# Performance work log

Hardware: AMD Instinct MI355X
Metric: run time of the kernel (lower is better)

## Reference

```python
import jax, jax.numpy as jnp
import numpy as np

B, EMBED, H, W = 16, 256, 64, 64
HEADS, POINTS = 8, 4  # mmcv MultiScaleDeformableAttention defaults, num_levels=1


def make_pe(d, h, w):
    # LoFTR-style PositionEncodingSine: pe[0::4]=sin(x*div), pe[1::4]=cos(x*div),
    # pe[2::4]=sin(y*div), pe[3::4]=cos(y*div); x,y are 1-based cumsum positions.
    y = jnp.broadcast_to(jnp.arange(1, h + 1, dtype=jnp.float32)[:, None], (h, w))
    x = jnp.broadcast_to(jnp.arange(1, w + 1, dtype=jnp.float32)[None, :], (h, w))
    div = jnp.exp(jnp.arange(0, d // 2, 2, dtype=jnp.float32) * (-np.log(10000.0) / (d // 2)))
    div = div[:, None, None]  # (d//4,1,1)
    pe = jnp.stack([jnp.sin(x * div), jnp.cos(x * div), jnp.sin(y * div), jnp.cos(y * div)], axis=1)
    return pe.reshape(d, h, w)[None]  # (1,d,h,w)


def reference_points(h, w):
    # Faithful to original: meshgrid(linspace(0,1,W), linspace(0,1,H), indexing='ij'),
    # stack (col, row), flatten -> (W*H, 2)
    gx, gy = jnp.meshgrid(jnp.linspace(0.0, 1.0, w), jnp.linspace(0.0, 1.0, h), indexing='ij')
    return jnp.stack([gy, gx], -1).reshape(-1, 2)


def reference(query, value, W_off, b_off, W_attn, b_attn, W_val, b_val, W_out, b_out):
    Bq, C, h, w = query.shape
    N = h * w
    d = C // HEADS
    pe = make_pe(C, h, w)
    q = query + pe  # query += self.pe(query)
    q_flat = q.reshape(Bq, C, N).transpose(0, 2, 1)      # (B,N,C)
    v_flat = value.reshape(Bq, C, N).transpose(0, 2, 1)  # (B,N,C)
    # value projection, split heads: (B,heads,N,d) -- spatial index n = y*w + x
    v = (v_flat @ W_val.T + b_val).reshape(Bq, N, HEADS, d).transpose(0, 2, 1, 3)
    off = (q_flat @ W_off.T + b_off).reshape(Bq, N, HEADS, POINTS, 2)
    attn = jax.nn.softmax((q_flat @ W_attn.T + b_attn).reshape(Bq, N, HEADS, POINTS), axis=-1)
    ref = reference_points(h, w)                          # (N,2)
    normalizer = jnp.array([w, h], jnp.float32)           # (W, H) per mmcv
    loc = ref[None, :, None, None, :] + off / normalizer  # (B,N,heads,P,2) in [0,1]
    grid = 2.0 * loc - 1.0                                # grid_sample coords, align_corners=False
    sx = grid[..., 0].transpose(0, 2, 1, 3).reshape(Bq, HEADS, N * POINTS)
    sy = grid[..., 1].transpose(0, 2, 1, 3).reshape(Bq, HEADS, N * POINTS)
    ix = (sx + 1.0) * w * 0.5 - 0.5
    iy = (sy + 1.0) * h * 0.5 - 0.5
    x0f = jnp.floor(ix); y0f = jnp.floor(iy)
    wx = ix - x0f; wy = iy - y0f
    x0 = x0f.astype(jnp.int32); y0 = y0f.astype(jnp.int32)

    def gather(yi, xi):
        # zero padding outside the image
        valid = (xi >= 0) & (xi < w) & (yi >= 0) & (yi < h)
        idx = jnp.clip(yi, 0, h - 1) * w + jnp.clip(xi, 0, w - 1)  # (B,heads,M)
        g = jnp.take_along_axis(v, idx[..., None], axis=2)          # (B,heads,M,d)
        return g * valid[..., None]

    samp = (((1 - wx) * (1 - wy))[..., None] * gather(y0, x0)
            + (wx * (1 - wy))[..., None] * gather(y0, x0 + 1)
            + ((1 - wx) * wy)[..., None] * gather(y0 + 1, x0)
            + (wx * wy)[..., None] * gather(y0 + 1, x0 + 1))        # (B,heads,N*P,d)
    samp = samp.reshape(Bq, HEADS, N, POINTS, d)
    attn_t = attn.transpose(0, 2, 1, 3)                             # (B,heads,N,P)
    out = jnp.einsum('bhnp,bhnpd->bnhd', attn_t, samp).reshape(Bq, N, C)
    out = out @ W_out.T + b_out + q_flat  # mmcv internal identity residual (dropout in eval = id)
    out = out.transpose(0, 2, 1).reshape(Bq, C, h, w)
    return out + q  # outer residual: output + query (query already has pe added)


def setup_inputs():
    key = jax.random.key(0)
    ks = jax.random.split(key, 8)
    s = 0.02
    return {
        'query': jax.random.normal(ks[0], (B, EMBED, H, W), jnp.float32),
        'value': jax.random.normal(ks[1], (B, EMBED, H, W), jnp.float32),
        'W_off': jax.random.normal(ks[2], (HEADS * POINTS * 2, EMBED), jnp.float32) * s,
        'b_off': jax.random.normal(ks[3], (HEADS * POINTS * 2,), jnp.float32) * 2.0,
        'W_attn': jax.random.normal(ks[4], (HEADS * POINTS, EMBED), jnp.float32) * s,
        'b_attn': jnp.zeros((HEADS * POINTS,), jnp.float32),
        'W_val': jax.random.normal(ks[5], (EMBED, EMBED), jnp.float32) * s,
        'b_val': jnp.zeros((EMBED,), jnp.float32),
        'W_out': jax.random.normal(ks[6], (EMBED, EMBED), jnp.float32) * s,
        'b_out': jnp.zeros((EMBED,), jnp.float32),
    }
```

## Files before the change

kernel.cpp:

```cpp
#include <hip/hip_runtime.h>
#include <hip/hip_bf16.h>

typedef __bf16 bf16;
typedef bf16 bf16x8 __attribute__((ext_vector_type(8)));
typedef bf16 bf16x4 __attribute__((ext_vector_type(4)));
typedef float f32x4 __attribute__((ext_vector_type(4)));

#define CB 16
#define CC 256
#define CH 64
#define CW 64
#define CN 4096
#define NHEADS 8
#define NPOINTS 4
#define HDIM 32
#define TBP 132

#define MFMA16(a, b, c) __builtin_amdgcn_mfma_f32_16x16x32_bf16(a, b, c, 0, 0, 0)

__device__ __forceinline__ void gload16(const void* g, void* l) {
    __builtin_amdgcn_global_load_lds((const __attribute__((address_space(1))) void*)g,
                                     (__attribute__((address_space(3))) void*)l, 16, 0, 0);
}

__global__ __launch_bounds__(256) void pe_pack(float* __restrict__ pe,
                                               const float* __restrict__ Wv,
                                               const float* __restrict__ Woff,
                                               const float* __restrict__ Wattn,
                                               const float* __restrict__ Wout,
                                               bf16* __restrict__ Wv_bf,
                                               bf16* __restrict__ W96_bf,
                                               bf16* __restrict__ Wout_bf) {
    int idx = blockIdx.x * 256 + threadIdx.x;
    if (idx < CC * CN) {
        int c = idx >> 12, n = idx & (CN - 1);
        int r = n >> 6, x = n & 63;
        int i = c >> 2, t = c & 3;
        float div = __expf(-logf(10000.0f) * (float)i / 64.0f);
        float arg = ((t < 2) ? (float)(x + 1) : (float)(r + 1)) * div;
        pe[idx] = (t & 1) ? cosf(arg) : sinf(arg);
    }
    if (idx < CC * CC) {
        Wv_bf[idx] = (bf16)Wv[idx];
        Wout_bf[idx] = (bf16)Wout[idx];
    }
    if (idx < 96 * CC) {
        W96_bf[idx] = (bf16)((idx < 64 * CC) ? Woff[idx] : Wattn[idx - 64 * CC]);
    }
}

__global__ __launch_bounds__(256) void vproj_g(const float* __restrict__ value,
                                               const bf16* __restrict__ Wv,
                                               const float* __restrict__ bv,
                                               bf16* __restrict__ v_s) {
    __shared__ __align__(16) char smem[17408];
    float* T = (float*)smem;
    const int TP = 66;

    int tid = threadIdx.x, lane = tid & 63, wave = tid >> 6;
    int wm = wave >> 1, wn = wave & 1, g = lane >> 4, lr = lane & 15;
    int n0 = blockIdx.x * 64, m0 = blockIdx.y * 128, b = blockIdx.z;
    int nl = tid & 63, kg = tid >> 6;
    const float* src = value + (size_t)b * CC * CN + n0 + nl;

    float v[16];
#pragma unroll
    for (int p = 0; p < 16; ++p) v[p] = src[(size_t)(kg * 16 + p) * CN];

    f32x4 acc[4][2] = {};
    for (int t = 0; t < 4; ++t) {
#pragma unroll
        for (int half = 0; half < 2; ++half) {
            bf16x8 o;
#pragma unroll
            for (int p = 0; p < 8; ++p) o[p] = (bf16)v[half * 8 + p];
            int slot = (kg * 2 + half) ^ (nl & 7);
            *(bf16x8*)(smem + (t & 1) * 8192 + nl * 128 + slot * 16) = o;
        }
        __syncthreads();
        if (t < 3) {
#pragma unroll
            for (int p = 0; p < 16; ++p)
                v[p] = src[(size_t)((t + 1) * 64 + kg * 16 + p) * CN];
        }
#pragma unroll
        for (int ks = 0; ks < 2; ++ks) {
            bf16x8 af[4], bfr[2];
#pragma unroll
            for (int mf = 0; mf < 4; ++mf)
                af[mf] = *(const bf16x8*)&Wv[(size_t)(m0 + wm * 64 + mf * 16 + lr) * CC + t * 64 + ks * 32 + g * 8];
#pragma unroll
            for (int nf = 0; nf < 2; ++nf) {
                int row = wn * 32 + nf * 16 + lr;
                bfr[nf] = *(const bf16x8*)(smem + (t & 1) * 8192 + row * 128 + (((ks * 4 + g) ^ (row & 7)) * 16));
            }
#pragma unroll
            for (int mf = 0; mf < 4; ++mf)
#pragma unroll
                for (int nf = 0; nf < 2; ++nf)
                    acc[mf][nf] = MFMA16(af[mf], bfr[nf], acc[mf][nf]);
        }
    }

#pragma unroll
    for (int pass = 0; pass < 2; ++pass) {
        __syncthreads();
        if (wm == pass) {
#pragma unroll
            for (int mf = 0; mf < 4; ++mf)
#pragma unroll
                for (int nf = 0; nf < 2; ++nf)
#pragma unroll
                    for (int i = 0; i < 4; ++i)
                        T[(mf * 16 + g * 4 + i) * TP + wn * 32 + nf * 16 + lr] = acc[mf][nf][i];
        }
        __syncthreads();
#pragma unroll
        for (int it = 0; it < 2; ++it) {
            int item = it * 256 + tid;
            int qg = item & 7, n_l = item >> 3;
            int cg = m0 + pass * 64 + qg * 8;
            int head = cg >> 5, dd0 = cg & 31;
            bf16x8 o;
#pragma unroll
            for (int u = 0; u < 8; ++u)
                o[u] = (bf16)(T[(qg * 8 + u) * TP + n_l] + bv[cg + u]);
            *(bf16x8*)&v_s[(((size_t)b * NHEADS + head) * CN + n0 + n_l) * HDIM + dd0] = o;
        }
    }
}

__global__ __launch_bounds__(256, 4) void offattn_sample(const float* __restrict__ query,
                                                         const float* __restrict__ pe,
                                                         const bf16* __restrict__ W96,
                                                         const float* __restrict__ boff,
                                                         const float* __restrict__ battn,
                                                         const bf16* __restrict__ v_s,
                                                         bf16* __restrict__ s) {
    __shared__ __align__(16) char smem[33792];
    float* ot = (float*)smem;
    unsigned* tbl = (unsigned*)smem;

    int tid = threadIdx.x, lane = tid & 63, wave = tid >> 6;
    int wm = wave >> 1, wn = wave & 1, g = lane >> 4, lr = lane & 15;
    int id = blockIdx.x;
    int xcd = id & 7, local = id >> 3;
    int b = xcd * 2 + (local >> 6);
    int nt = local & 63;
    int n0 = nt * 64;
    int nl = tid & 63, kg = tid >> 6;
    const float* qs = query + (size_t)b * CC * CN + n0 + nl;
    const float* ps = pe + n0 + nl;

    float v[16];
#pragma unroll
    for (int p = 0; p < 16; ++p) {
        size_t off = (size_t)(kg * 16 + p) * CN;
        v[p] = __builtin_nontemporal_load(&qs[off]) + ps[off];
    }
    asm volatile("" ::: "memory");

    f32x4 acc[3][2] = {};
    for (int t = 0; t < 4; ++t) {
#pragma unroll
        for (int half = 0; half < 2; ++half) {
            bf16x8 o;
#pragma unroll
            for (int p = 0; p < 8; ++p) o[p] = (bf16)v[half * 8 + p];
            int slot = (kg * 2 + half) ^ (nl & 7);
            *(bf16x8*)(smem + (t & 1) * 8192 + nl * 128 + slot * 16) = o;
        }
        __syncthreads();
        if (t < 3) {
#pragma unroll
            for (int p = 0; p < 16; ++p) {
                size_t off = (size_t)((t + 1) * 64 + kg * 16 + p) * CN;
                v[p] = __builtin_nontemporal_load(&qs[off]) + ps[off];
            }
            asm volatile("" ::: "memory");
        }
#pragma unroll
        for (int ks = 0; ks < 2; ++ks) {
            bf16x8 af[3], bfr[2];
#pragma unroll
            for (int mf = 0; mf < 3; ++mf)
                af[mf] = *(const bf16x8*)&W96[(size_t)(wm * 48 + mf * 16 + lr) * CC + t * 64 + ks * 32 + g * 8];
#pragma unroll
            for (int nf = 0; nf < 2; ++nf) {
                int row = wn * 32 + nf * 16 + lr;
                bfr[nf] = *(const bf16x8*)(smem + (t & 1) * 8192 + row * 128 + (((ks * 4 + g) ^ (row & 7)) * 16));
            }
#pragma unroll
            for (int mf = 0; mf < 3; ++mf)
#pragma unroll
                for (int nf = 0; nf < 2; ++nf)
                    acc[mf][nf] = MFMA16(af[mf], bfr[nf], acc[mf][nf]);
        }
    }
    __syncthreads();

#pragma unroll
    for (int mf = 0; mf < 3; ++mf) {
#pragma unroll
        for (int i = 0; i < 4; ++i) {
            int j = wm * 48 + mf * 16 + g * 4 + i;
            float bias = (j < 64) ? boff[j] : battn[j - 64];
#pragma unroll
            for (int nf = 0; nf < 2; ++nf) {
                int col = wn * 32 + nf * 16 + lr;
                ot[j * 65 + col] = acc[mf][nf][i] + bias;
            }
        }
    }
    __syncthreads();

    unsigned pk[2][16];
#pragma unroll
    for (int it = 0; it < 2; ++it) {
        int item = it * 256 + tid;
        int inl = item & 63, h = item >> 6;
        float lg0 = ot[(64 + h * 4 + 0) * 65 + inl];
        float lg1 = ot[(64 + h * 4 + 1) * 65 + inl];
        float lg2 = ot[(64 + h * 4 + 2) * 65 + inl];
        float lg3 = ot[(64 + h * 4 + 3) * 65 + inl];
        float m = fmaxf(fmaxf(lg0, lg1), fmaxf(lg2, lg3));
        float e0 = __expf(lg0 - m), e1 = __expf(lg1 - m);
        float e2 = __expf(lg2 - m), e3 = __expf(lg3 - m);
        float inv = 1.0f / (e0 + e1 + e2 + e3);
        float ep[4] = {e0, e1, e2, e3};
#pragma unroll
        for (int p = 0; p < NPOINTS; ++p) {
            float off0 = ot[(h * 8 + p * 2 + 0) * 65 + inl];
            float off1 = ot[(h * 8 + p * 2 + 1) * 65 + inl];
            float ix = (float)inl * (64.0f / 63.0f) + off0 - 0.5f;
            float iy = (float)nt * (64.0f / 63.0f) + off1 - 0.5f;
            float x0f = floorf(ix), y0f = floorf(iy);
            float wx = ix - x0f, wy = iy - y0f;
            int x0 = (int)x0f, y0 = (int)y0f;
            int x1 = x0 + 1, y1 = y0 + 1;
            float vx0 = (x0 >= 0 && x0 < CW) ? 1.f : 0.f;
            float vx1 = (x1 >= 0 && x1 < CW) ? 1.f : 0.f;
            float vy0 = (y0 >= 0 && y0 < CH) ? 1.f : 0.f;
            float vy1 = (y1 >= 0 && y1 < CH) ? 1.f : 0.f;
            int x0c = min(max(x0, 0), CW - 1), x1c = min(max(x1, 0), CW - 1);
            int y0c = min(max(y0, 0), CH - 1), y1c = min(max(y1, 0), CH - 1);
            float a = ep[p] * inv;
            float w00 = a * (1.f - wx) * (1.f - wy) * vx0 * vy0;
            float w01 = a * wx * (1.f - wy) * vx1 * vy0;
            float w10 = a * (1.f - wx) * wy * vx0 * vy1;
            float w11 = a * wx * wy * vx1 * vy1;
            unsigned c00 = (unsigned)(y0c * CW + x0c), c01 = (unsigned)(y0c * CW + x1c);
            unsigned c10 = (unsigned)(y1c * CW + x0c), c11 = (unsigned)(y1c * CW + x1c);
            pk[it][p * 4 + 0] = ((unsigned)__builtin_bit_cast(unsigned short, (_Float16)w00) << 16) | c00;
            pk[it][p * 4 + 1] = ((unsigned)__builtin_bit_cast(unsigned short, (_Float16)w01) << 16) | c01;
            pk[it][p * 4 + 2] = ((unsigned)__builtin_bit_cast(unsigned short, (_Float16)w10) << 16) | c10;
            pk[it][p * 4 + 3] = ((unsigned)__builtin_bit_cast(unsigned short, (_Float16)w11) << 16) | c11;
        }
    }
    __syncthreads();
#pragma unroll
    for (int it = 0; it < 2; ++it) {
        int item = it * 256 + tid;
        int inl = item & 63, h = item >> 6;
        uint4* dst = (uint4*)(tbl + inl * TBP + h * 16);
#pragma unroll
        for (int j = 0; j < 4; ++j) {
            uint4 w4;
            w4.x = pk[it][j * 4 + 0]; w4.y = pk[it][j * 4 + 1];
            w4.z = pk[it][j * 4 + 2]; w4.w = pk[it][j * 4 + 3];
            dst[j] = w4;
        }
    }
    __syncthreads();

    int q = tid & 3, h2 = (tid >> 2) & 7, ng = tid >> 5;
    const bf16* vb = v_s + (((size_t)b * NHEADS + h2) * CN) * HDIM + q * 8;
#pragma unroll
    for (int iter = 0; iter < 8; ++iter) {
        int snl = iter * 8 + ng;
        const uint4* tb4 = (const uint4*)(tbl + snl * TBP + h2 * 16);
        unsigned ue[16];
#pragma unroll
        for (int j = 0; j < 4; ++j) {
            uint4 t4 = tb4[j];
            ue[j * 4 + 0] = t4.x; ue[j * 4 + 1] = t4.y;
            ue[j * 4 + 2] = t4.z; ue[j * 4 + 3] = t4.w;
        }
        asm volatile("" ::: "memory");
        bf16x8 gr[16];
#pragma unroll
        for (int e = 0; e < 16; ++e)
            gr[e] = *(const bf16x8*)&vb[(int)(ue[e] & 0xFFFu) * HDIM];
        asm volatile("" ::: "memory");
        float a0 = 0.f, a1 = 0.f, a2 = 0.f, a3 = 0.f;
        float a4 = 0.f, a5 = 0.f, a6 = 0.f, a7 = 0.f;
#pragma unroll
        for (int e = 0; e < 16; ++e) {
            float w = (float)__builtin_bit_cast(_Float16, (unsigned short)(ue[e] >> 16));
            a0 += w * (float)gr[e][0]; a1 += w * (float)gr[e][1];
            a2 += w * (float)gr[e][2]; a3 += w * (float)gr[e][3];
            a4 += w * (float)gr[e][4]; a5 += w * (float)gr[e][5];
            a6 += w * (float)gr[e][6]; a7 += w * (float)gr[e][7];
        }
        bf16x8 o;
        o[0] = (bf16)a0; o[1] = (bf16)a1; o[2] = (bf16)a2; o[3] = (bf16)a3;
        o[4] = (bf16)a4; o[5] = (bf16)a5; o[6] = (bf16)a6; o[7] = (bf16)a7;
        *(bf16x8*)&s[((size_t)b * CN + n0 + snl) * CC + h2 * 32 + q * 8] = o;
    }
}

__global__ __launch_bounds__(256) void outproj_v8(const bf16* __restrict__ s_t,
                                                  const bf16* __restrict__ Wout,
                                                  const float* __restrict__ bout,
                                                  const float* __restrict__ query,
                                                  const float* __restrict__ pe,
                                                  float* __restrict__ out) {
    __shared__ __align__(16) char smem[33792];
    float* T = (float*)smem;
    const int TP = 132;

    int tid = threadIdx.x, lane = tid & 63, wave = tid >> 6;
    int wm = wave >> 1, wn = wave & 1, g = lane >> 4, lr = lane & 15;
    int id = blockIdx.x;
    int swz = (id & 7) * 128 + (id >> 3);
    int n0 = (swz & 31) * 128, c0 = ((swz >> 5) & 1) * 128, b = swz >> 6;
    const bf16* sb = s_t + ((size_t)b * CN + n0) * CC;

    int rloc = lane >> 2, sl = lane & 3;

    auto stage = [&](int t, int bsel) {
#pragma unroll
        for (int j = 0; j < 2; ++j) {
            int cidx = wave * 2 + j;
            int row = cidx * 16 + rloc;
            int chunk = sl ^ (row & 3);
            const bf16* gA = sb + (size_t)row * CC + t * 32 + chunk * 8;
            const bf16* gB = Wout + (size_t)(c0 + row) * CC + t * 32 + chunk * 8;
            gload16(gA, smem + bsel * 16384 + cidx * 1024);
            gload16(gB, smem + bsel * 16384 + 8192 + cidx * 1024);
        }
    };

    stage(0, 0);

    f32x4 acc[4][4] = {};
    for (int t = 0; t < 8; ++t) {
        __syncthreads();
        if (t < 7) stage(t + 1, (t + 1) & 1);
        bf16x8 af[4], bfr[4];
#pragma unroll
        for (int mf = 0; mf < 4; ++mf) {
            int row = wm * 64 + mf * 16 + lr;
            af[mf] = *(const bf16x8*)(smem + (t & 1) * 16384 + row * 64 + ((g ^ (row & 3)) * 16));
        }
#pragma unroll
        for (int nf = 0; nf < 4; ++nf) {
            int row = wn * 64 + nf * 16 + lr;
            bfr[nf] = *(const bf16x8*)(smem + (t & 1) * 16384 + 8192 + row * 64 + ((g ^ (row & 3)) * 16));
        }
#pragma unroll
        for (int mf = 0; mf < 4; ++mf)
#pragma unroll
            for (int nf = 0; nf < 4; ++nf)
                acc[mf][nf] = MFMA16(af[mf], bfr[nf], acc[mf][nf]);
    }
    __syncthreads();

    int lr5 = tid & 31, rq = tid >> 5;
#pragma unroll
    for (int ch = 0; ch < 2; ++ch) {
        if (wn == ch) {
#pragma unroll
            for (int mf = 0; mf < 4; ++mf)
#pragma unroll
                for (int nf = 0; nf < 4; ++nf) {
                    int cl = nf * 16 + lr;
                    int nl = wm * 64 + mf * 16 + g * 4;
                    *(f32x4*)&T[cl * TP + nl] = acc[mf][nf];
                }
        }
        __syncthreads();
#pragma unroll
        for (int pass = 0; pass < 8; ++pass) {
            int cl = pass * 8 + rq;
            int c = c0 + ch * 64 + cl;
            int n = n0 + lr5 * 4;
            f32x4 v = *(const f32x4*)&T[cl * TP + lr5 * 4];
            size_t base = ((size_t)b * CC + c) * CN + n;
            f32x4 q4 = *(const f32x4*)&query[base];
            f32x4 p4 = *(const f32x4*)&pe[(size_t)c * CN + n];
            float bias = bout[c];
#pragma unroll
            for (int j = 0; j < 4; ++j) v[j] = v[j] + bias + 2.0f * (q4[j] + p4[j]);
            *(f32x4*)&out[base] = v;
        }
        __syncthreads();
    }
}

extern "C" void kernel_launch(void* const* d_in, const int* in_sizes, int n_in,
                              void* d_out, int out_size, void* d_ws, size_t ws_size,
                              hipStream_t stream) {
    const float* query = (const float*)d_in[0];
    const float* value = (const float*)d_in[1];
    const float* W_off = (const float*)d_in[2];
    const float* b_off = (const float*)d_in[3];
    const float* W_attn = (const float*)d_in[4];
    const float* b_attn = (const float*)d_in[5];
    const float* W_val = (const float*)d_in[6];
    const float* b_val = (const float*)d_in[7];
    const float* W_out = (const float*)d_in[8];
    const float* b_out = (const float*)d_in[9];
    float* out = (float*)d_out;

    char* p = (char*)d_ws;
    float* pe = (float*)p;            p += (size_t)CC * CN * 4;
    bf16* Wv_bf = (bf16*)p;           p += (size_t)CC * CC * 2;
    bf16* Wout_bf = (bf16*)p;         p += (size_t)CC * CC * 2;
    bf16* W96_bf = (bf16*)p;          p += (size_t)96 * CC * 2 + 256;
    bf16* v_s = (bf16*)p;             p += (size_t)CB * NHEADS * CN * HDIM * 2;
    bf16* s_t = (bf16*)p;             p += (size_t)CB * CN * CC * 2;

    pe_pack<<<dim3((CC * CN + 255) / 256), dim3(256), 0, stream>>>(pe, W_val, W_off, W_attn,
                                                                   W_out, Wv_bf, W96_bf, Wout_bf);
    vproj_g<<<dim3(CN / 64, 2, CB), dim3(256), 0, stream>>>(value, Wv_bf, b_val, v_s);
    offattn_sample<<<dim3(1024), dim3(256), 0, stream>>>(query, pe, W96_bf,
                                                         b_off, b_attn, v_s, s_t);
    outproj_v8<<<dim3(1024), dim3(256), 0, stream>>>(s_t, Wout_bf, b_out, query, pe, out);
}
```

Baseline: 136.4 us.

## Merge value projection with offset/attention compute; split sampling into separate kernel

The value projection and the offset/attention-weight projection now run in one launch, selected by blockIdx.y, so the two independent GEMMs can execute concurrently on the GPU. The packed bilinear sampling table is written to a global buffer instead of shared memory, and a new kernel does the gather-and-accumulate sampling. This removes the serialization between the value projection and the offset computation. In exchange it adds a 32 MB global table that must be written and read back, plus an extra kernel launch.

```diff
diff --git a/kernel.cpp b/kernel.cpp
--- a/kernel.cpp
+++ b/kernel.cpp
@@ -14,7 +14,6 @@
 #define NHEADS 8
 #define NPOINTS 4
 #define HDIM 32
-#define TBP 132
 
 #define MFMA16(a, b, c) __builtin_amdgcn_mfma_f32_16x16x32_bf16(a, b, c, 0, 0, 0)
 
@@ -49,104 +48,98 @@
     }
 }
 
-__global__ __launch_bounds__(256) void vproj_g(const float* __restrict__ value,
-                                               const bf16* __restrict__ Wv,
-                                               const float* __restrict__ bv,
-                                               bf16* __restrict__ v_s) {
-    __shared__ __align__(16) char smem[17408];
-    float* T = (float*)smem;
-    const int TP = 66;
-
+__global__ __launch_bounds__(256) void vproj_oa(const float* __restrict__ value,
+                                                const bf16* __restrict__ Wv,
+                                                const float* __restrict__ bv,
+                                                bf16* __restrict__ v_s,
+                                                const float* __restrict__ query,
+                                                const float* __restrict__ pe,
+                                                const bf16* __restrict__ W96,
+                                                const float* __restrict__ boff,
+                                                const float* __restrict__ battn,
+                                                unsigned* __restrict__ tbl_g) {
+    __shared__ __align__(16) char smem[33792];
     int tid = threadIdx.x, lane = tid & 63, wave = tid >> 6;
     int wm = wave >> 1, wn = wave & 1, g = lane >> 4, lr = lane & 15;
-    int n0 = blockIdx.x * 64, m0 = blockIdx.y * 128, b = blockIdx.z;
-    int nl = tid & 63, kg = tid >> 6;
-    const float* src = value + (size_t)b * CC * CN + n0 + nl;
-
-    float v[16];
-#pragma unroll
-    for (int p = 0; p < 16; ++p) v[p] = src[(size_t)(kg * 16 + p) * CN];
-
-    f32x4 acc[4][2] = {};
-    for (int t = 0; t < 4; ++t) {
-#pragma unroll
-        for (int half = 0; half < 2; ++half) {
-            bf16x8 o;
-#pragma unroll
-            for (int p = 0; p < 8; ++p) o[p] = (bf16)v[half * 8 + p];
-            int slot = (kg * 2 + half) ^ (nl & 7);
-            *(bf16x8*)(smem + (t & 1) * 8192 + nl * 128 + slot * 16) = o;
-        }
-        __syncthreads();
-        if (t < 3) {
-#pragma unroll
-            for (int p = 0; p < 16; ++p)
-                v[p] = src[(size_t)((t + 1) * 64 + kg * 16 + p) * CN];
-        }
-#pragma unroll
-        for (int ks = 0; ks < 2; ++ks) {
-            bf16x8 af[4], bfr[2];
-#pragma unroll
-            for (int mf = 0; mf < 4; ++mf)
-                af[mf] = *(const bf16x8*)&Wv[(size_t)(m0 + wm * 64 + mf * 16 + lr) * CC + t * 64 + ks * 32 + g * 8];
-#pragma unroll
-            for (int nf = 0; nf < 2; ++nf) {
-                int row = wn * 32 + nf * 16 + lr;
-                bfr[nf] = *(const bf16x8*)(smem + (t & 1) * 8192 + row * 128 + (((ks * 4 + g) ^ (row & 7)) * 16));
-            }
-#pragma unroll
-            for (int mf = 0; mf < 4; ++mf)
-#pragma unroll
-                for (int nf = 0; nf < 2; ++nf)
-                    acc[mf][nf] = MFMA16(af[mf], bfr[nf], acc[mf][nf]);
-        }
-    }
-
-#pragma unroll
-    for (int pass = 0; pass < 2; ++pass) {
-        __syncthreads();
-        if (wm == pass) {
-#pragma unroll
-            for (int mf = 0; mf < 4; ++mf)
-#pragma unroll
-                for (int nf = 0; nf < 2; ++nf)
-#pragma unroll
-                    for (int i = 0; i < 4; ++i)
-                        T[(mf * 16 + g * 4 + i) * TP + wn * 32 + nf * 16 + lr] = acc[mf][nf][i];
-        }
-        __syncthreads();
-#pragma unroll
-        for (int it = 0; it < 2; ++it) {
-            int item = it * 256 + tid;
-            int qg = item & 7, n_l = item >> 3;
-            int cg = m0 + pass * 64 + qg * 8;
-            int head = cg >> 5, dd0 = cg & 31;
-            bf16x8 o;
-#pragma unroll
-            for (int u = 0; u < 8; ++u)
-                o[u] = (bf16)(T[(qg * 8 + u) * TP + n_l] + bv[cg + u]);
-            *(bf16x8*)&v_s[(((size_t)b * NHEADS + head) * CN + n0 + n_l) * HDIM + dd0] = o;
-        }
-    }
-}
-
-__global__ __launch_bounds__(256, 4) void offattn_sample(const float* __restrict__ query,
-                                                         const float* __restrict__ pe,
-                                                         const bf16* __restrict__ W96,
-                                                         const float* __restrict__ boff,
-                                                         const float* __restrict__ battn,
-                                                         const bf16* __restrict__ v_s,
-                                                         bf16* __restrict__ s) {
-    __shared__ __align__(16) char smem[33792];
+    int b = blockIdx.z;
+
+    if (blockIdx.y < 2) {
+        float* T = (float*)smem;
+        const int TP = 66;
+        int n0 = blockIdx.x * 64, m0 = blockIdx.y * 128;
+        int nl = tid & 63, kg = tid >> 6;
+        const float* src = value + (size_t)b * CC * CN + n0 + nl;
+
+        float v[16];
+#pragma unroll
+        for (int p = 0; p < 16; ++p) v[p] = src[(size_t)(kg * 16 + p) * CN];
+
+        f32x4 acc[4][2] = {};
+        for (int t = 0; t < 4; ++t) {
+#pragma unroll
+            for (int half = 0; half < 2; ++half) {
+                bf16x8 o;
+#pragma unroll
+                for (int p = 0; p < 8; ++p) o[p] = (bf16)v[half * 8 + p];
+                int slot = (kg * 2 + half) ^ (nl & 7);
+                *(bf16x8*)(smem + (t & 1) * 8192 + nl * 128 + slot * 16) = o;
+            }
+            __syncthreads();
+            if (t < 3) {
+#pragma unroll
+                for (int p = 0; p < 16; ++p)
+                    v[p] = src[(size_t)((t + 1) * 64 + kg * 16 + p) * CN];
+            }
+#pragma unroll
+            for (int ks = 0; ks < 2; ++ks) {
+                bf16x8 af[4], bfr[2];
+#pragma unroll
+                for (int mf = 0; mf < 4; ++mf)
+                    af[mf] = *(const bf16x8*)&Wv[(size_t)(m0 + wm * 64 + mf * 16 + lr) * CC + t * 64 + ks * 32 + g * 8];
+#pragma unroll
+                for (int nf = 0; nf < 2; ++nf) {
+                    int row = wn * 32 + nf * 16 + lr;
+                    bfr[nf] = *(const bf16x8*)(smem + (t & 1) * 8192 + row * 128 + (((ks * 4 + g) ^ (row & 7)) * 16));
+                }
+#pragma unroll
+                for (int mf = 0; mf < 4; ++mf)
+#pragma unroll
+                    for (int nf = 0; nf < 2; ++nf)
+                        acc[mf][nf] = MFMA16(af[mf], bfr[nf], acc[mf][nf]);
+            }
+        }
+
+#pragma unroll
+        for (int pass = 0; pass < 2; ++pass) {
+            __syncthreads();
+            if (wm == pass) {
+#pragma unroll
+                for (int mf = 0; mf < 4; ++mf)
+#pragma unroll
+                    for (int nf = 0; nf < 2; ++nf)
+#pragma unroll
+                        for (int i = 0; i < 4; ++i)
+                            T[(mf * 16 + g * 4 + i) * TP + wn * 32 + nf * 16 + lr] = acc[mf][nf][i];
+            }
+            __syncthreads();
+#pragma unroll
+            for (int it = 0; it < 2; ++it) {
+                int item = it * 256 + tid;
+                int qg = item & 7, n_l = item >> 3;
+                int cg = m0 + pass * 64 + qg * 8;
+                int head = cg >> 5, dd0 = cg & 31;
+                bf16x8 o;
+#pragma unroll
+                for (int u = 0; u < 8; ++u)
+                    o[u] = (bf16)(T[(qg * 8 + u) * TP + n_l] + bv[cg + u]);
+                *(bf16x8*)&v_s[(((size_t)b * NHEADS + head) * CN + n0 + n_l) * HDIM + dd0] = o;
+            }
+        }
+        return;
+    }
+
     float* ot = (float*)smem;
-    unsigned* tbl = (unsigned*)smem;
-
-    int tid = threadIdx.x, lane = tid & 63, wave = tid >> 6;
-    int wm = wave >> 1, wn = wave & 1, g = lane >> 4, lr = lane & 15;
-    int id = blockIdx.x;
-    int xcd = id & 7, local = id >> 3;
-    int b = xcd * 2 + (local >> 6);
-    int nt = local & 63;
+    int nt = blockIdx.x;
     int n0 = nt * 64;
     int nl = tid & 63, kg = tid >> 6;
     const float* qs = query + (size_t)b * CC * CN + n0 + nl;
@@ -214,11 +207,10 @@
     }
     __syncthreads();
 
-    unsigned pk[2][16];
 #pragma unroll
     for (int it = 0; it < 2; ++it) {
         int item = it * 256 + tid;
-        int inl = item & 63, h = item >> 6;
+        int h = item & 7, inl = item >> 3;
         float lg0 = ot[(64 + h * 4 + 0) * 65 + inl];
         float lg1 = ot[(64 + h * 4 + 1) * 65 + inl];
         float lg2 = ot[(64 + h * 4 + 2) * 65 + inl];
@@ -228,6 +220,7 @@
         float e2 = __expf(lg2 - m), e3 = __expf(lg3 - m);
         float inv = 1.0f / (e0 + e1 + e2 + e3);
         float ep[4] = {e0, e1, e2, e3};
+        uint4* dst = (uint4*)(tbl_g + ((size_t)b * CN + n0 + inl) * 128 + h * 16);
 #pragma unroll
         for (int p = 0; p < NPOINTS; ++p) {
             float off0 = ot[(h * 8 + p * 2 + 0) * 65 + inl];
@@ -249,36 +242,31 @@
             float w01 = a * wx * (1.f - wy) * vx1 * vy0;
             float w10 = a * (1.f - wx) * wy * vx0 * vy1;
             float w11 = a * wx * wy * vx1 * vy1;
-            unsigned c00 = (unsigned)(y0c * CW + x0c), c01 = (unsigned)(y0c * CW + x1c);
-            unsigned c10 = (unsigned)(y1c * CW + x0c), c11 = (unsigned)(y1c * CW + x1c);
-            pk[it][p * 4 + 0] = ((unsigned)__builtin_bit_cast(unsigned short, (_Float16)w00) << 16) | c00;
-            pk[it][p * 4 + 1] = ((unsigned)__builtin_bit_cast(unsigned short, (_Float16)w01) << 16) | c01;
-            pk[it][p * 4 + 2] = ((unsigned)__builtin_bit_cast(unsigned short, (_Float16)w10) << 16) | c10;
-            pk[it][p * 4 + 3] = ((unsigned)__builtin_bit_cast(unsigned short, (_Float16)w11) << 16) | c11;
-        }
-    }
-    __syncthreads();
-#pragma unroll
-    for (int it = 0; it < 2; ++it) {
-        int item = it * 256 + tid;
-        int inl = item & 63, h = item >> 6;
-        uint4* dst = (uint4*)(tbl + inl * TBP + h * 16);
-#pragma unroll
-        for (int j = 0; j < 4; ++j) {
             uint4 w4;
-            w4.x = pk[it][j * 4 + 0]; w4.y = pk[it][j * 4 + 1];
-            w4.z = pk[it][j * 4 + 2]; w4.w = pk[it][j * 4 + 3];
-            dst[j] = w4;
-        }
-    }
-    __syncthreads();
-
+            w4.x = ((unsigned)__builtin_bit_cast(unsigned short, (_Float16)w00) << 16) | (unsigned)(y0c * CW + x0c);
+            w4.y = ((unsigned)__builtin_bit_cast(unsigned short, (_Float16)w01) << 16) | (unsigned)(y0c * CW + x1c);
+            w4.z = ((unsigned)__builtin_bit_cast(unsigned short, (_Float16)w10) << 16) | (unsigned)(y1c * CW + x0c);
+            w4.w = ((unsigned)__builtin_bit_cast(unsigned short, (_Float16)w11) << 16) | (unsigned)(y1c * CW + x1c);
+            dst[p] = w4;
+        }
+    }
+}
+
+__global__ __launch_bounds__(256, 4) void sample_k(const unsigned* __restrict__ tbl_g,
+                                                   const bf16* __restrict__ v_s,
+                                                   bf16* __restrict__ s) {
+    int tid = threadIdx.x;
+    int id = blockIdx.x;
+    int xcd = id & 7, local = id >> 3;
+    int b = xcd * 2 + (local >> 6);
+    int nt = local & 63;
+    int n0 = nt * 64;
     int q = tid & 3, h2 = (tid >> 2) & 7, ng = tid >> 5;
     const bf16* vb = v_s + (((size_t)b * NHEADS + h2) * CN) * HDIM + q * 8;
 #pragma unroll
     for (int iter = 0; iter < 8; ++iter) {
         int snl = iter * 8 + ng;
-        const uint4* tb4 = (const uint4*)(tbl + snl * TBP + h2 * 16);
+        const uint4* tb4 = (const uint4*)(tbl_g + ((size_t)b * CN + n0 + snl) * 128 + h2 * 16);
         unsigned ue[16];
 #pragma unroll
         for (int j = 0; j < 4; ++j) {
@@ -420,11 +408,13 @@
     bf16* W96_bf = (bf16*)p;          p += (size_t)96 * CC * 2 + 256;
     bf16* v_s = (bf16*)p;             p += (size_t)CB * NHEADS * CN * HDIM * 2;
     bf16* s_t = (bf16*)p;             p += (size_t)CB * CN * CC * 2;
+    unsigned* tbl_g = (unsigned*)p;   p += (size_t)CB * CN * 128 * 4;
 
     pe_pack<<<dim3((CC * CN + 255) / 256), dim3(256), 0, stream>>>(pe, W_val, W_off, W_attn,
                                                                    W_out, Wv_bf, W96_bf, Wout_bf);
-    vproj_g<<<dim3(CN / 64, 2, CB), dim3(256), 0, stream>>>(value, Wv_bf, b_val, v_s);
-    offattn_sample<<<dim3(1024), dim3(256), 0, stream>>>(query, pe, W96_bf,
-                                                         b_off, b_attn, v_s, s_t);
+    vproj_oa<<<dim3(CN / 64, 3, CB), dim3(256), 0, stream>>>(value, Wv_bf, b_val, v_s,
+                                                             query, pe, W96_bf, b_off, b_attn,
+                                                             tbl_g);
+    sample_k<<<dim3(1024), dim3(256), 0, stream>>>(tbl_g, v_s, s_t);
     outproj_v8<<<dim3(1024), dim3(256), 0, stream>>>(s_t, Wout_bf, b_out, query, pe, out);
 }
```

Measured after the change: 154.9 us. 1.14x slower.
